# Kernel optimization log

Measured on AMD Instinct MI355X. Metric: run time of the kernel, lower is better.

Reference implementation:

```python
import jax, jax.numpy as jnp
import numpy as np
from functools import partial

HID = 256
HOR = 5

def _lin(k, i, o):
    return jax.random.normal(k, (i, o), jnp.float32) / np.sqrt(i)

def setup_inputs() -> dict:
    key = jax.random.key(0)
    ks = jax.random.split(key, 32)
    B, T, D, Hf, Wf = 4, 16, 768, 16, 16
    H, W = 1024, 1024
    inp = {}
    inp['features'] = jax.random.normal(ks[0], (B, T, D, Hf, Wf), jnp.float32)
    inp['predictions'] = jax.random.uniform(ks[1], (B, T, 1, H, W), dtype=jnp.float32)
    # position encoder: 4 -> HID -> HID
    inp['pe_w1'] = _lin(ks[2], 4, HID); inp['pe_b1'] = jnp.zeros((HID,), jnp.float32)
    inp['pe_w2'] = _lin(ks[3], HID, HID); inp['pe_b2'] = jnp.zeros((HID,), jnp.float32)
    # 2-layer LSTM, gate order i,f,g,o (torch convention)
    inp['wih0'] = _lin(ks[4], HID, 4 * HID); inp['whh0'] = _lin(ks[5], HID, 4 * HID)
    inp['bih0'] = jnp.zeros((4 * HID,), jnp.float32); inp['bhh0'] = jnp.zeros((4 * HID,), jnp.float32)
    inp['wih1'] = _lin(ks[6], HID, 4 * HID); inp['whh1'] = _lin(ks[7], HID, 4 * HID)
    inp['bih1'] = jnp.zeros((4 * HID,), jnp.float32); inp['bhh1'] = jnp.zeros((4 * HID,), jnp.float32)
    # motion predictor: HID -> HID -> HID/2 -> HOR*4
    inp['mp_w1'] = _lin(ks[8], HID, HID); inp['mp_b1'] = jnp.zeros((HID,), jnp.float32)
    inp['mp_w2'] = _lin(ks[9], HID, HID // 2); inp['mp_b2'] = jnp.zeros((HID // 2,), jnp.float32)
    inp['mp_w3'] = _lin(ks[10], HID // 2, HOR * 4); inp['mp_b3'] = jnp.zeros((HOR * 4,), jnp.float32)
    # confidence: HID -> HID/2 -> HOR
    inp['cf_w1'] = _lin(ks[11], HID, HID // 2); inp['cf_b1'] = jnp.zeros((HID // 2,), jnp.float32)
    inp['cf_w2'] = _lin(ks[12], HID // 2, HOR); inp['cf_b2'] = jnp.zeros((HOR,), jnp.float32)
    return inp

def _extract_bboxes(predictions):
    # predictions: (B,T,1,H,W) -> bboxes (B,T,4) in (cx,cy,w,h), normalized
    B, T, _, H, W = predictions.shape
    mask = predictions[:, :, 0] > 0.5  # (B,T,H,W)
    xs = jnp.arange(W, dtype=jnp.float32)           # (W,)
    ys = jnp.arange(H, dtype=jnp.float32)[:, None]  # (H,1)
    big = jnp.float32(H + W)
    x_min = jnp.min(jnp.where(mask, xs, big), axis=(-2, -1))
    x_max = jnp.max(jnp.where(mask, xs, -1.0), axis=(-2, -1))
    y_min = jnp.min(jnp.where(mask, ys, big), axis=(-2, -1))
    y_max = jnp.max(jnp.where(mask, ys, -1.0), axis=(-2, -1))
    has = jnp.any(mask, axis=(-2, -1))  # (B,T)
    cx = (x_min + x_max) / 2.0 / W
    cy = (y_min + y_max) / 2.0 / H
    w = (x_max - x_min) / W
    h = (y_max - y_min) / H
    bbox = jnp.stack([cx, cy, w, h], axis=-1)  # (B,T,4)
    default = jnp.array([0.5, 0.5, 0.1, 0.1], dtype=jnp.float32)
    return jnp.where(has[..., None], bbox, default)

def _lstm_layer(x, wih, whh, bih, bhh):
    # x: (B,T,HID); returns (hs (B,T,H), h_final (B,H))
    B = x.shape[0]
    xg = jnp.einsum('bti,ig->btg', x, wih) + bih  # (B,T,4H)
    def step(carry, xg_t):
        h, c = carry
        g = xg_t + h @ whh + bhh
        i, f, gg, o = jnp.split(g, 4, axis=-1)
        i = jax.nn.sigmoid(i); f = jax.nn.sigmoid(f)
        gg = jnp.tanh(gg); o = jax.nn.sigmoid(o)
        c = f * c + i * gg
        h = o * jnp.tanh(c)
        return (h, c), h
    z = jnp.zeros((B, HID), x.dtype)
    (h, c), hs = jax.lax.scan(step, (z, z), xg.swapaxes(0, 1))
    return hs.swapaxes(0, 1), h

def reference(features, predictions, pe_w1, pe_b1, pe_w2, pe_b2,
              wih0, whh0, bih0, bhh0, wih1, whh1, bih1, bhh1,
              mp_w1, mp_b1, mp_w2, mp_b2, mp_w3, mp_b3,
              cf_w1, cf_b1, cf_w2, cf_b2):
    B, T = features.shape[:2]
    bboxes = _extract_bboxes(predictions)  # (B,T,4)
    pos = jax.nn.relu(bboxes @ pe_w1 + pe_b1)
    pos = jax.nn.relu(pos @ pe_w2 + pe_b2)  # (B,T,HID)
    h1, _ = _lstm_layer(pos, wih0, whh0, bih0, bhh0)
    motion_features, last_hidden = _lstm_layer(h1, wih1, whh1, bih1, bhh1)
    x = jax.nn.relu(last_hidden @ mp_w1 + mp_b1)
    x = jax.nn.relu(x @ mp_w2 + mp_b2)
    predicted_deltas = (x @ mp_w3 + mp_b3).reshape(B, HOR, 4)
    last_bbox = bboxes[:, -1:, :]
    predicted_bboxes = last_bbox + jnp.cumsum(predicted_deltas, axis=1)
    c = jax.nn.relu(last_hidden @ cf_w1 + cf_b1)
    confidence = jax.nn.sigmoid(c @ cf_w2 + cf_b2)  # (B,HOR)
    predicted_locations = predicted_bboxes[..., :2]
    predicted_scales = predicted_bboxes[..., 2:]
    return (predicted_deltas, predicted_bboxes, predicted_locations,
            predicted_scales, motion_features, confidence, bboxes)
```

## Files before the change

### kernel.cpp

```cpp
#include <hip/hip_runtime.h>
#include <math.h>

#define BIGI (1 << 30)

#define PM_OFF    0
#define HT0_OFF   8192
#define HT2_OFF   40960
#define XG1_OFF   45056
#define ZERO_BEG  8192
#define ZERO_END  176128

#define OUT_DELTAS 0
#define OUT_PBB    80
#define OUT_LOC    160
#define OUT_SCL    200
#define OUT_MF     240
#define OUT_CONF   16624
#define OUT_BBOX   16644

__device__ __forceinline__ float sigmoidf_(float x) { return 1.0f / (1.0f + expf(-x)); }

__device__ __forceinline__ void storeh(unsigned long long* p, float h, int tag) {
    unsigned long long v =
        ((unsigned long long)(unsigned)tag << 32) | (unsigned long long)__float_as_uint(h);
    __hip_atomic_store(p, v, __ATOMIC_RELAXED, __HIP_MEMORY_SCOPE_AGENT);
}
__device__ __forceinline__ float pollh(const unsigned long long* p, int tag) {
    unsigned long long v = __hip_atomic_load(p, __ATOMIC_RELAXED, __HIP_MEMORY_SCOPE_AGENT);
    while ((int)(v >> 32) != tag) {
        __builtin_amdgcn_s_sleep(1);
        v = __hip_atomic_load(p, __ATOMIC_RELAXED, __HIP_MEMORY_SCOPE_AGENT);
    }
    return __uint_as_float((unsigned)v);
}

__global__ __launch_bounds__(256) void k_minmax(const float4* __restrict__ pred,
                                                int* __restrict__ ws) {
    int tid = threadIdx.x;
    {
        int i = ZERO_BEG + blockIdx.x * 256 + tid;
        if (i < ZERO_END) ws[i] = 0;
    }
    int img = blockIdx.x >> 5;
    int chunk = blockIdx.x & 31;
    int base = img * 262144 + chunk * 8192 + tid;
    int xmn = BIGI, xmx = -1, ymn = BIGI, ymx = -1;
#pragma unroll 4
    for (int i = 0; i < 32; ++i) {
        int idx4 = base + i * 256;
        float4 v = pred[idx4];
        int x = (idx4 << 2) & 1023;
        int y = (idx4 >> 8) & 1023;
        bool m0 = v.x > 0.5f, m1 = v.y > 0.5f, m2 = v.z > 0.5f, m3 = v.w > 0.5f;
        int cmn = m0 ? x : (m1 ? x + 1 : (m2 ? x + 2 : (m3 ? x + 3 : BIGI)));
        int cmx = m3 ? x + 3 : (m2 ? x + 2 : (m1 ? x + 1 : (m0 ? x : -1)));
        xmn = min(xmn, cmn);
        xmx = max(xmx, cmx);
        if (m0 | m1 | m2 | m3) { ymn = min(ymn, y); ymx = max(ymx, y); }
    }
    for (int off = 32; off > 0; off >>= 1) {
        xmn = min(xmn, __shfl_down(xmn, off));
        xmx = max(xmx, __shfl_down(xmx, off));
        ymn = min(ymn, __shfl_down(ymn, off));
        ymx = max(ymx, __shfl_down(ymx, off));
    }
    __shared__ int red[4][4];
    int wave = tid >> 6;
    if ((tid & 63) == 0) { red[0][wave] = xmn; red[1][wave] = xmx; red[2][wave] = ymn; red[3][wave] = ymx; }
    __syncthreads();
    if (tid == 0) {
        xmn = min(min(red[0][0], red[0][1]), min(red[0][2], red[0][3]));
        xmx = max(max(red[1][0], red[1][1]), max(red[1][2], red[1][3]));
        ymn = min(min(red[2][0], red[2][1]), min(red[2][2], red[2][3]));
        ymx = max(max(red[3][0], red[3][1]), max(red[3][2], red[3][3]));
        ((int4*)(ws + PM_OFF))[blockIdx.x] = make_int4(xmn, xmx, ymn, ymx);
    }
}

__device__ __forceinline__ void mk_bbox(int xmn, int xmx, int ymn, int ymx, float* o) {
    if (xmx >= 0) {
        o[0] = (float)(xmn + xmx) * (0.5f / 1024.0f);
        o[1] = (float)(ymn + ymx) * (0.5f / 1024.0f);
        o[2] = (float)(xmx - xmn) * (1.0f / 1024.0f);
        o[3] = (float)(ymx - ymn) * (1.0f / 1024.0f);
    } else { o[0] = 0.5f; o[1] = 0.5f; o[2] = 0.1f; o[3] = 0.1f; }
}

__global__ __launch_bounds__(512, 2) void k_fused(
    const float* __restrict__ pe_w1, const float* __restrict__ pe_b1,
    const float* __restrict__ pe_w2, const float* __restrict__ pe_b2,
    const float* __restrict__ wih0, const float* __restrict__ whh0,
    const float* __restrict__ bih0, const float* __restrict__ bhh0,
    const float* __restrict__ wih1, const float* __restrict__ whh1,
    const float* __restrict__ bih1, const float* __restrict__ bhh1,
    const float* __restrict__ mp_w1, const float* __restrict__ mp_b1,
    const float* __restrict__ mp_w2, const float* __restrict__ mp_b2,
    const float* __restrict__ mp_w3, const float* __restrict__ mp_b3,
    const float* __restrict__ cf_w1, const float* __restrict__ cf_b1,
    const float* __restrict__ cf_w2, const float* __restrict__ cf_b2,
    const int4* __restrict__ pm4, unsigned long long* __restrict__ hT0,
    unsigned long long* __restrict__ hT2, unsigned long long* __restrict__ xg1,
    float* __restrict__ out) {
    __shared__ __align__(16) float sA[4096];
    __shared__ __align__(16) float sB[4096];
    __shared__ __align__(16) float hsm[256];
    __shared__ float xsm[256];
    __shared__ float partA[512];
    __shared__ float sBB[64];
    const int tid = threadIdx.x, blk = blockIdx.x;
    const int stage = blk >> 4;
    const int b = (blk >> 2) & 3, g = blk & 3;
    const int c = tid & 255, kh = tid >> 8;
    const int col = ((c >> 6) << 8) + g * 64 + (c & 63);
    const int krow0 = kh * 128;

    float4 wreg[32];
    float cst = 0.0f;

    if (stage == 0) {
        {
            int il = tid >> 5, ch = tid & 31;
            int4 v = pm4[(b * 16 + il) * 32 + ch];
            int xmn = v.x, xmx = v.y, ymn = v.z, ymx = v.w;
            for (int off = 16; off > 0; off >>= 1) {
                xmn = min(xmn, __shfl_down(xmn, off, 32));
                xmx = max(xmx, __shfl_down(xmx, off, 32));
                ymn = min(ymn, __shfl_down(ymn, off, 32));
                ymx = max(ymx, __shfl_down(ymx, off, 32));
            }
            if (ch == 0) {
                float bb[4];
                mk_bbox(xmn, xmx, ymn, ymx, bb);
                sBB[il * 4 + 0] = bb[0]; sBB[il * 4 + 1] = bb[1];
                sBB[il * 4 + 2] = bb[2]; sBB[il * 4 + 3] = bb[3];
                if (g == 0) {
                    out[OUT_BBOX + (b * 16 + il) * 4 + 0] = bb[0];
                    out[OUT_BBOX + (b * 16 + il) * 4 + 1] = bb[1];
                    out[OUT_BBOX + (b * 16 + il) * 4 + 2] = bb[2];
                    out[OUT_BBOX + (b * 16 + il) * 4 + 3] = bb[3];
                }
            }
        }
        __syncthreads();
        if (tid < 256) {
            float w0 = pe_w1[tid], w1 = pe_w1[256 + tid];
            float w2 = pe_w1[512 + tid], w3 = pe_w1[768 + tid], b1v = pe_b1[tid];
#pragma unroll
            for (int i = 0; i < 16; ++i) {
                float v = sBB[i * 4] * w0 + sBB[i * 4 + 1] * w1 +
                          sBB[i * 4 + 2] * w2 + sBB[i * 4 + 3] * w3 + b1v;
                sB[i * 256 + tid] = fmaxf(v, 0.0f);
            }
        }
        __syncthreads();
        {
            int i0 = kh * 8;
            float acc[8];
            float b2v = pe_b2[c];
#pragma unroll
            for (int i = 0; i < 8; ++i) acc[i] = b2v;
            for (int k = 0; k < 256; ++k) {
                float wv = pe_w2[k * 256 + c];
#pragma unroll
                for (int i = 0; i < 8; ++i) acc[i] += sB[(i0 + i) * 256 + k] * wv;
            }
#pragma unroll
            for (int i = 0; i < 8; ++i) sA[(i0 + i) * 256 + c] = fmaxf(acc[i], 0.0f);
        }
        __syncthreads();
#pragma unroll
        for (int k4 = 0; k4 < 32; ++k4) {
            int r = krow0 + k4 * 4;
            wreg[k4].x = wih0[(r + 0) * 1024 + col];
            wreg[k4].y = wih0[(r + 1) * 1024 + col];
            wreg[k4].z = wih0[(r + 2) * 1024 + col];
            wreg[k4].w = wih0[(r + 3) * 1024 + col];
        }
        float xacc[16];
#pragma unroll
        for (int t = 0; t < 16; ++t) {
            const float4* pr = (const float4*)&sA[t * 256 + krow0];
            float a = 0.0f;
#pragma unroll
            for (int k = 0; k < 32; ++k) {
                float4 x = pr[k];
                a += x.x * wreg[k].x + x.y * wreg[k].y + x.z * wreg[k].z + x.w * wreg[k].w;
            }
            xacc[t] = a;
        }
        if (kh == 1) {
#pragma unroll
            for (int t = 0; t < 16; ++t) sB[t * 256 + c] = xacc[t];
        }
        __syncthreads();
        if (kh == 0) {
            float bsum = bih0[col] + bhh0[col];
#pragma unroll
            for (int t = 0; t < 16; ++t) sB[t * 256 + c] = xacc[t] + sB[t * 256 + c] + bsum;
        }
        __syncthreads();
#pragma unroll
        for (int k4 = 0; k4 < 32; ++k4) {
            int r = krow0 + k4 * 4;
            wreg[k4].x = whh0[(r + 0) * 1024 + col];
            wreg[k4].y = whh0[(r + 1) * 1024 + col];
            wreg[k4].z = whh0[(r + 2) * 1024 + col];
            wreg[k4].w = whh0[(r + 3) * 1024 + col];
        }
        for (int t = 0; t < 16; ++t) {
            if (t && tid < 256) hsm[tid] = pollh(&hT0[((b * 16 + t - 1) << 8) + tid], t);
            __syncthreads();
            float a = 0.0f;
            if (t) {
                const float4* hr = (const float4*)&hsm[krow0];
#pragma unroll
                for (int k = 0; k < 32; ++k) {
                    float4 h = hr[k];
                    a += h.x * wreg[k].x + h.y * wreg[k].y + h.z * wreg[k].z + h.w * wreg[k].w;
                }
            }
            partA[kh * 256 + c] = a;
            __syncthreads();
            if (tid < 64) {
                int u = tid, unit = g * 64 + u;
                float gi = sB[t * 256 + u]       + partA[u]       + partA[256 + u];
                float gf = sB[t * 256 + 64 + u]  + partA[64 + u]  + partA[320 + u];
                float gg = sB[t * 256 + 128 + u] + partA[128 + u] + partA[384 + u];
                float go = sB[t * 256 + 192 + u] + partA[192 + u] + partA[448 + u];
                float i_ = sigmoidf_(gi), f_ = sigmoidf_(gf);
                float g_ = tanhf(gg), o_ = sigmoidf_(go);
                cst = f_ * cst + i_ * g_;
                float h = o_ * tanhf(cst);
                storeh(&hT0[((b * 16 + t) << 8) + unit], h, t + 1);
            }
        }
        return;
    }

    if (stage == 1) {
#pragma unroll
        for (int k4 = 0; k4 < 32; ++k4) {
            int r = krow0 + k4 * 4;
            wreg[k4].x = wih1[(r + 0) * 1024 + col];
            wreg[k4].y = wih1[(r + 1) * 1024 + col];
            wreg[k4].z = wih1[(r + 2) * 1024 + col];
            wreg[k4].w = wih1[(r + 3) * 1024 + col];
        }
        float bsum = 0.0f;
        if (tid < 256) bsum = bih1[col] + bhh1[col];
        for (int t = 0; t < 16; ++t) {
            if (tid < 256) hsm[tid] = pollh(&hT0[((b * 16 + t) << 8) + tid], t + 1);
            __syncthreads();
            const float4* hr = (const float4*)&hsm[krow0];
            float a = 0.0f;
#pragma unroll
            for (int k = 0; k < 32; ++k) {
                float4 h = hr[k];
                a += h.x * wreg[k].x + h.y * wreg[k].y + h.z * wreg[k].z + h.w * wreg[k].w;
            }
            partA[kh * 256 + c] = a;
            __syncthreads();
            if (tid < 256) {
                float v = partA[tid] + partA[256 + tid] + bsum;
                storeh(&xg1[((b * 16 + t) << 10) + col], v, t + 1);
            }
        }
        return;
    }

#pragma unroll
    for (int k4 = 0; k4 < 32; ++k4) {
        int r = krow0 + k4 * 4;
        wreg[k4].x = whh1[(r + 0) * 1024 + col];
        wreg[k4].y = whh1[(r + 1) * 1024 + col];
        wreg[k4].z = whh1[(r + 2) * 1024 + col];
        wreg[k4].w = whh1[(r + 3) * 1024 + col];
    }
    for (int t = 0; t < 16; ++t) {
        if (tid < 256) {
            if (t) hsm[tid] = pollh(&hT2[(((b << 1) | ((t - 1) & 1)) << 8) + tid], t);
        } else {
            int cc = tid - 256;
            int colx = ((cc >> 6) << 8) + g * 64 + (cc & 63);
            xsm[cc] = pollh(&xg1[((b * 16 + t) << 10) + colx], t + 1);
        }
        __syncthreads();
        float a = 0.0f;
        if (t) {
            const float4* hr = (const float4*)&hsm[krow0];
#pragma unroll
            for (int k = 0; k < 32; ++k) {
                float4 h = hr[k];
                a += h.x * wreg[k].x + h.y * wreg[k].y + h.z * wreg[k].z + h.w * wreg[k].w;
            }
        }
        partA[kh * 256 + c] = a;
        __syncthreads();
        if (tid < 64) {
            int u = tid, unit = g * 64 + u;
            float gi = xsm[u]       + partA[u]       + partA[256 + u];
            float gf = xsm[64 + u]  + partA[64 + u]  + partA[320 + u];
            float gg = xsm[128 + u] + partA[128 + u] + partA[384 + u];
            float go = xsm[192 + u] + partA[192 + u] + partA[448 + u];
            float i_ = sigmoidf_(gi), f_ = sigmoidf_(gf);
            float g_ = tanhf(gg), o_ = sigmoidf_(go);
            cst = f_ * cst + i_ * g_;
            float h = o_ * tanhf(cst);
            storeh(&hT2[(((b << 1) | (t & 1)) << 8) + unit], h, t + 1);
            out[OUT_MF + (b * 16 + t) * 256 + unit] = h;
        }
    }
    if (g != 0) return;

    float* lh = sA;
    float* x1 = sA + 256;
    float* c1 = sA + 512;
    float* x2 = sA + 640;
    float* dl = sA + 768;
    if (tid < 256) lh[tid] = pollh(&hT2[(((b << 1) | 1) << 8) + tid], 16);
    if (tid < 32) {
        int4 v = pm4[(b * 16 + 15) * 32 + tid];
        int xmn = v.x, xmx = v.y, ymn = v.z, ymx = v.w;
        for (int off = 16; off > 0; off >>= 1) {
            xmn = min(xmn, __shfl_down(xmn, off, 32));
            xmx = max(xmx, __shfl_down(xmx, off, 32));
            ymn = min(ymn, __shfl_down(ymn, off, 32));
            ymx = max(ymx, __shfl_down(ymx, off, 32));
        }
        if (tid == 0) mk_bbox(xmn, xmx, ymn, ymx, sBB);
    }
    __syncthreads();
    if (tid < 256) {
        float a = mp_b1[tid];
#pragma unroll 4
        for (int k = 0; k < 256; ++k) a += lh[k] * mp_w1[k * 256 + tid];
        x1[tid] = fmaxf(a, 0.0f);
    } else if (tid < 384) {
        int jj = tid - 256;
        float a = cf_b1[jj];
#pragma unroll 4
        for (int k = 0; k < 256; ++k) a += lh[k] * cf_w1[k * 128 + jj];
        c1[jj] = fmaxf(a, 0.0f);
    }
    __syncthreads();
    if (tid < 128) {
        float a = mp_b2[tid];
#pragma unroll 4
        for (int k = 0; k < 256; ++k) a += x1[k] * mp_w2[k * 128 + tid];
        x2[tid] = fmaxf(a, 0.0f);
    } else if (tid >= 256 && tid < 261) {
        int jj = tid - 256;
        float a = cf_b2[jj];
#pragma unroll 4
        for (int k = 0; k < 128; ++k) a += c1[k] * cf_w2[k * 5 + jj];
        out[OUT_CONF + b * 5 + jj] = sigmoidf_(a);
    }
    __syncthreads();
    if (tid < 20) {
        float a = mp_b3[tid];
#pragma unroll 4
        for (int k = 0; k < 128; ++k) a += x2[k] * mp_w3[k * 20 + tid];
        dl[tid] = a;
        out[OUT_DELTAS + b * 20 + tid] = a;
    }
    __syncthreads();
    if (tid < 4) {
        float acc = sBB[tid];
        for (int hh = 0; hh < 5; ++hh) {
            acc += dl[hh * 4 + tid];
            out[OUT_PBB + b * 20 + hh * 4 + tid] = acc;
            if (tid < 2) out[OUT_LOC + b * 10 + hh * 2 + tid] = acc;
            else out[OUT_SCL + b * 10 + hh * 2 + (tid - 2)] = acc;
        }
    }
}

extern "C" void kernel_launch(void* const* d_in, const int* in_sizes, int n_in,
                              void* d_out, int out_size, void* d_ws, size_t ws_size,
                              hipStream_t stream) {
    (void)in_sizes; (void)n_in; (void)out_size; (void)ws_size;
    const float* pred = (const float*)d_in[1];
    const float* pe_w1 = (const float*)d_in[2];
    const float* pe_b1 = (const float*)d_in[3];
    const float* pe_w2 = (const float*)d_in[4];
    const float* pe_b2 = (const float*)d_in[5];
    const float* wih0 = (const float*)d_in[6];
    const float* whh0 = (const float*)d_in[7];
    const float* bih0 = (const float*)d_in[8];
    const float* bhh0 = (const float*)d_in[9];
    const float* wih1 = (const float*)d_in[10];
    const float* whh1 = (const float*)d_in[11];
    const float* bih1 = (const float*)d_in[12];
    const float* bhh1 = (const float*)d_in[13];
    const float* mp_w1 = (const float*)d_in[14];
    const float* mp_b1 = (const float*)d_in[15];
    const float* mp_w2 = (const float*)d_in[16];
    const float* mp_b2 = (const float*)d_in[17];
    const float* mp_w3 = (const float*)d_in[18];
    const float* mp_b3 = (const float*)d_in[19];
    const float* cf_w1 = (const float*)d_in[20];
    const float* cf_b1 = (const float*)d_in[21];
    const float* cf_w2 = (const float*)d_in[22];
    const float* cf_b2 = (const float*)d_in[23];
    float* out = (float*)d_out;
    int* wsi = (int*)d_ws;

    hipLaunchKernelGGL(k_minmax, dim3(64 * 32), dim3(256), 0, stream,
                       (const float4*)pred, wsi);
    hipLaunchKernelGGL(k_fused, dim3(48), dim3(512), 0, stream,
                       pe_w1, pe_b1, pe_w2, pe_b2,
                       wih0, whh0, bih0, bhh0,
                       wih1, whh1, bih1, bhh1,
                       mp_w1, mp_b1, mp_w2, mp_b2, mp_w3, mp_b3,
                       cf_w1, cf_b1, cf_w2, cf_b2,
                       (const int4*)(wsi + PM_OFF),
                       (unsigned long long*)(wsi + HT0_OFF),
                       (unsigned long long*)(wsi + HT2_OFF),
                       (unsigned long long*)(wsi + XG1_OFF),
                       out);
}
```

Baseline: 559.5 us.

## Split fused LSTM kernel across twice as many smaller blocks per batch

Repartitions the fused LSTM pipeline from 48 blocks of 512 threads to 96 blocks of 256 threads, each owning 32 hidden units per gate instead of 64. The K dimension is still split into two halves across threads, and the per-block gate work, shared buffers and bbox reduction are resized to match. Layer-1 x-gates and the recurrent hidden state are now polled together in one helper, and the confidence head is moved into otherwise idle threads. The aim is more CUs working on each recurrent step with less work per block, at the cost of more cross-block polling traffic and more blocks to synchronise each timestep.

New measurement: 570.0 us. About the same (+1.9%).

```diff
diff --git a/kernel.cpp b/kernel.cpp
--- a/kernel.cpp
+++ b/kernel.cpp
@@ -32,6 +32,20 @@
         v = __hip_atomic_load(p, __ATOMIC_RELAXED, __HIP_MEMORY_SCOPE_AGENT);
     }
     return __uint_as_float((unsigned)v);
+}
+__device__ __forceinline__ float2 pollh2(const unsigned long long* p1, int tag1,
+                                         const unsigned long long* p2, int tag2) {
+    unsigned long long v1 = __hip_atomic_load(p1, __ATOMIC_RELAXED, __HIP_MEMORY_SCOPE_AGENT);
+    unsigned long long v2 = __hip_atomic_load(p2, __ATOMIC_RELAXED, __HIP_MEMORY_SCOPE_AGENT);
+    while ((int)(v1 >> 32) != tag1) {
+        __builtin_amdgcn_s_sleep(1);
+        v1 = __hip_atomic_load(p1, __ATOMIC_RELAXED, __HIP_MEMORY_SCOPE_AGENT);
+    }
+    while ((int)(v2 >> 32) != tag2) {
+        __builtin_amdgcn_s_sleep(1);
+        v2 = __hip_atomic_load(p2, __ATOMIC_RELAXED, __HIP_MEMORY_SCOPE_AGENT);
+    }
+    return make_float2(__uint_as_float((unsigned)v1), __uint_as_float((unsigned)v2));
 }
 
 __global__ __launch_bounds__(256) void k_minmax(const float4* __restrict__ pred,
@@ -86,7 +100,7 @@
     } else { o[0] = 0.5f; o[1] = 0.5f; o[2] = 0.1f; o[3] = 0.1f; }
 }
 
-__global__ __launch_bounds__(512, 2) void k_fused(
+__global__ __launch_bounds__(256, 1) void k_fused(
     const float* __restrict__ pe_w1, const float* __restrict__ pe_b1,
     const float* __restrict__ pe_w2, const float* __restrict__ pe_b2,
     const float* __restrict__ wih0, const float* __restrict__ whh0,
@@ -103,15 +117,16 @@
     float* __restrict__ out) {
     __shared__ __align__(16) float sA[4096];
     __shared__ __align__(16) float sB[4096];
+    __shared__ float xgl[2048];
     __shared__ __align__(16) float hsm[256];
-    __shared__ float xsm[256];
-    __shared__ float partA[512];
+    __shared__ float xsm[128];
+    __shared__ float part[256];
     __shared__ float sBB[64];
     const int tid = threadIdx.x, blk = blockIdx.x;
-    const int stage = blk >> 4;
-    const int b = (blk >> 2) & 3, g = blk & 3;
-    const int c = tid & 255, kh = tid >> 8;
-    const int col = ((c >> 6) << 8) + g * 64 + (c & 63);
+    const int stage = blk >> 5;
+    const int b = (blk >> 3) & 3, g = blk & 7;
+    const int j = tid & 127, kh = tid >> 7;
+    const int col = ((j >> 5) << 8) + g * 32 + (j & 31);
     const int krow0 = kh * 128;
 
     float4 wreg[32];
@@ -119,16 +134,18 @@
 
     if (stage == 0) {
         {
-            int il = tid >> 5, ch = tid & 31;
-            int4 v = pm4[(b * 16 + il) * 32 + ch];
-            int xmn = v.x, xmx = v.y, ymn = v.z, ymx = v.w;
-            for (int off = 16; off > 0; off >>= 1) {
-                xmn = min(xmn, __shfl_down(xmn, off, 32));
-                xmx = max(xmx, __shfl_down(xmx, off, 32));
-                ymn = min(ymn, __shfl_down(ymn, off, 32));
-                ymx = max(ymx, __shfl_down(ymx, off, 32));
-            }
-            if (ch == 0) {
+            int il = tid >> 4, c2 = (tid & 15) * 2;
+            int4 A = pm4[(b * 16 + il) * 32 + c2];
+            int4 B = pm4[(b * 16 + il) * 32 + c2 + 1];
+            int xmn = min(A.x, B.x), xmx = max(A.y, B.y);
+            int ymn = min(A.z, B.z), ymx = max(A.w, B.w);
+            for (int off = 8; off > 0; off >>= 1) {
+                xmn = min(xmn, __shfl_down(xmn, off, 16));
+                xmx = max(xmx, __shfl_down(xmx, off, 16));
+                ymn = min(ymn, __shfl_down(ymn, off, 16));
+                ymx = max(ymx, __shfl_down(ymx, off, 16));
+            }
+            if ((tid & 15) == 0) {
                 float bb[4];
                 mk_bbox(xmn, xmx, ymn, ymx, bb);
                 sBB[il * 4 + 0] = bb[0]; sBB[il * 4 + 1] = bb[1];
@@ -142,7 +159,7 @@
             }
         }
         __syncthreads();
-        if (tid < 256) {
+        {
             float w0 = pe_w1[tid], w1 = pe_w1[256 + tid];
             float w2 = pe_w1[512 + tid], w3 = pe_w1[768 + tid], b1v = pe_b1[tid];
 #pragma unroll
@@ -154,18 +171,17 @@
         }
         __syncthreads();
         {
-            int i0 = kh * 8;
-            float acc[8];
-            float b2v = pe_b2[c];
-#pragma unroll
-            for (int i = 0; i < 8; ++i) acc[i] = b2v;
+            float acc[16];
+            float b2v = pe_b2[tid];
+#pragma unroll
+            for (int i = 0; i < 16; ++i) acc[i] = b2v;
             for (int k = 0; k < 256; ++k) {
-                float wv = pe_w2[k * 256 + c];
-#pragma unroll
-                for (int i = 0; i < 8; ++i) acc[i] += sB[(i0 + i) * 256 + k] * wv;
-            }
-#pragma unroll
-            for (int i = 0; i < 8; ++i) sA[(i0 + i) * 256 + c] = fmaxf(acc[i], 0.0f);
+                float wv = pe_w2[k * 256 + tid];
+#pragma unroll
+                for (int i = 0; i < 16; ++i) acc[i] += sB[i * 256 + k] * wv;
+            }
+#pragma unroll
+            for (int i = 0; i < 16; ++i) sA[i * 256 + tid] = fmaxf(acc[i], 0.0f);
         }
         __syncthreads();
 #pragma unroll
@@ -176,29 +192,31 @@
             wreg[k4].z = wih0[(r + 2) * 1024 + col];
             wreg[k4].w = wih0[(r + 3) * 1024 + col];
         }
-        float xacc[16];
-#pragma unroll
-        for (int t = 0; t < 16; ++t) {
-            const float4* pr = (const float4*)&sA[t * 256 + krow0];
-            float a = 0.0f;
-#pragma unroll
-            for (int k = 0; k < 32; ++k) {
-                float4 x = pr[k];
-                a += x.x * wreg[k].x + x.y * wreg[k].y + x.z * wreg[k].z + x.w * wreg[k].w;
-            }
-            xacc[t] = a;
-        }
-        if (kh == 1) {
-#pragma unroll
-            for (int t = 0; t < 16; ++t) sB[t * 256 + c] = xacc[t];
-        }
-        __syncthreads();
-        if (kh == 0) {
+        {
+            float xacc[16];
+#pragma unroll
+            for (int t = 0; t < 16; ++t) {
+                const float4* pr = (const float4*)&sA[t * 256 + krow0];
+                float a = 0.0f;
+#pragma unroll
+                for (int k = 0; k < 32; ++k) {
+                    float4 x = pr[k];
+                    a += x.x * wreg[k].x + x.y * wreg[k].y + x.z * wreg[k].z + x.w * wreg[k].w;
+                }
+                xacc[t] = a;
+            }
+#pragma unroll
+            for (int t = 0; t < 16; ++t) sB[kh * 2048 + t * 128 + j] = xacc[t];
+        }
+        __syncthreads();
+        {
             float bsum = bih0[col] + bhh0[col];
-#pragma unroll
-            for (int t = 0; t < 16; ++t) sB[t * 256 + c] = xacc[t] + sB[t * 256 + c] + bsum;
-        }
-        __syncthreads();
+            int th = tid >> 7;
+            for (int i = 0; i < 8; ++i) {
+                int t = th + 2 * i;
+                xgl[t * 128 + j] = sB[t * 128 + j] + sB[2048 + t * 128 + j] + bsum;
+            }
+        }
 #pragma unroll
         for (int k4 = 0; k4 < 32; ++k4) {
             int r = krow0 + k4 * 4;
@@ -207,8 +225,9 @@
             wreg[k4].z = whh0[(r + 2) * 1024 + col];
             wreg[k4].w = whh0[(r + 3) * 1024 + col];
         }
+        __syncthreads();
         for (int t = 0; t < 16; ++t) {
-            if (t && tid < 256) hsm[tid] = pollh(&hT0[((b * 16 + t - 1) << 8) + tid], t);
+            if (t) hsm[tid] = pollh(&hT0[((b * 16 + t - 1) << 8) + tid], t);
             __syncthreads();
             float a = 0.0f;
             if (t) {
@@ -219,19 +238,19 @@
                     a += h.x * wreg[k].x + h.y * wreg[k].y + h.z * wreg[k].z + h.w * wreg[k].w;
                 }
             }
-            partA[kh * 256 + c] = a;
+            part[tid] = a;
             __syncthreads();
-            if (tid < 64) {
-                int u = tid, unit = g * 64 + u;
-                float gi = sB[t * 256 + u]       + partA[u]       + partA[256 + u];
-                float gf = sB[t * 256 + 64 + u]  + partA[64 + u]  + partA[320 + u];
-                float gg = sB[t * 256 + 128 + u] + partA[128 + u] + partA[384 + u];
-                float go = sB[t * 256 + 192 + u] + partA[192 + u] + partA[448 + u];
+            if (tid < 32) {
+                int u = tid;
+                float gi = xgl[t * 128 + u]      + part[u]       + part[128 + u];
+                float gf = xgl[t * 128 + 32 + u] + part[32 + u]  + part[160 + u];
+                float gg = xgl[t * 128 + 64 + u] + part[64 + u]  + part[192 + u];
+                float go = xgl[t * 128 + 96 + u] + part[96 + u]  + part[224 + u];
                 float i_ = sigmoidf_(gi), f_ = sigmoidf_(gf);
                 float g_ = tanhf(gg), o_ = sigmoidf_(go);
                 cst = f_ * cst + i_ * g_;
                 float h = o_ * tanhf(cst);
-                storeh(&hT0[((b * 16 + t) << 8) + unit], h, t + 1);
+                storeh(&hT0[((b * 16 + t) << 8) + g * 32 + u], h, t + 1);
             }
         }
         return;
@@ -246,10 +265,9 @@
             wreg[k4].z = wih1[(r + 2) * 1024 + col];
             wreg[k4].w = wih1[(r + 3) * 1024 + col];
         }
-        float bsum = 0.0f;
-        if (tid < 256) bsum = bih1[col] + bhh1[col];
+        float bsum = (tid < 128) ? (bih1[col] + bhh1[col]) : 0.0f;
         for (int t = 0; t < 16; ++t) {
-            if (tid < 256) hsm[tid] = pollh(&hT0[((b * 16 + t) << 8) + tid], t + 1);
+            hsm[tid] = pollh(&hT0[((b * 16 + t) << 8) + tid], t + 1);
             __syncthreads();
             const float4* hr = (const float4*)&hsm[krow0];
             float a = 0.0f;
@@ -258,12 +276,10 @@
                 float4 h = hr[k];
                 a += h.x * wreg[k].x + h.y * wreg[k].y + h.z * wreg[k].z + h.w * wreg[k].w;
             }
-            partA[kh * 256 + c] = a;
+            part[tid] = a;
             __syncthreads();
-            if (tid < 256) {
-                float v = partA[tid] + partA[256 + tid] + bsum;
-                storeh(&xg1[((b * 16 + t) << 10) + col], v, t + 1);
-            }
+            if (tid < 128)
+                storeh(&xg1[((b * 16 + t) << 10) + col], part[tid] + part[128 + tid] + bsum, t + 1);
         }
         return;
     }
@@ -277,12 +293,16 @@
         wreg[k4].w = whh1[(r + 3) * 1024 + col];
     }
     for (int t = 0; t < 16; ++t) {
-        if (tid < 256) {
-            if (t) hsm[tid] = pollh(&hT2[(((b << 1) | ((t - 1) & 1)) << 8) + tid], t);
-        } else {
-            int cc = tid - 256;
-            int colx = ((cc >> 6) << 8) + g * 64 + (cc & 63);
-            xsm[cc] = pollh(&xg1[((b * 16 + t) << 10) + colx], t + 1);
+        if (tid < 128) {
+            if (t) {
+                float2 v = pollh2(&xg1[((b * 16 + t) << 10) + col], t + 1,
+                                  &hT2[(((b << 1) | ((t - 1) & 1)) << 8) + tid], t);
+                xsm[tid] = v.x; hsm[tid] = v.y;
+            } else {
+                xsm[tid] = pollh(&xg1[((b * 16) << 10) + col], 1);
+            }
+        } else if (t) {
+            hsm[tid] = pollh(&hT2[(((b << 1) | ((t - 1) & 1)) << 8) + tid], t);
         }
         __syncthreads();
         float a = 0.0f;
@@ -294,14 +314,14 @@
                 a += h.x * wreg[k].x + h.y * wreg[k].y + h.z * wreg[k].z + h.w * wreg[k].w;
             }
         }
-        partA[kh * 256 + c] = a;
-        __syncthreads();
-        if (tid < 64) {
-            int u = tid, unit = g * 64 + u;
-            float gi = xsm[u]       + partA[u]       + partA[256 + u];
-            float gf = xsm[64 + u]  + partA[64 + u]  + partA[320 + u];
-            float gg = xsm[128 + u] + partA[128 + u] + partA[384 + u];
-            float go = xsm[192 + u] + partA[192 + u] + partA[448 + u];
+        part[tid] = a;
+        __syncthreads();
+        if (tid < 32) {
+            int u = tid, unit = g * 32 + u;
+            float gi = xsm[u]      + part[u]       + part[128 + u];
+            float gf = xsm[32 + u] + part[32 + u]  + part[160 + u];
+            float gg = xsm[64 + u] + part[64 + u]  + part[192 + u];
+            float go = xsm[96 + u] + part[96 + u]  + part[224 + u];
             float i_ = sigmoidf_(gi), f_ = sigmoidf_(gf);
             float g_ = tanhf(gg), o_ = sigmoidf_(go);
             cst = f_ * cst + i_ * g_;
@@ -317,7 +337,7 @@
     float* c1 = sA + 512;
     float* x2 = sA + 640;
     float* dl = sA + 768;
-    if (tid < 256) lh[tid] = pollh(&hT2[(((b << 1) | 1) << 8) + tid], 16);
+    lh[tid] = pollh(&hT2[(((b << 1) | 1) << 8) + tid], 16);
     if (tid < 32) {
         int4 v = pm4[(b * 16 + 15) * 32 + tid];
         int xmn = v.x, xmx = v.y, ymn = v.z, ymx = v.w;
@@ -330,17 +350,11 @@
         if (tid == 0) mk_bbox(xmn, xmx, ymn, ymx, sBB);
     }
     __syncthreads();
-    if (tid < 256) {
+    {
         float a = mp_b1[tid];
 #pragma unroll 4
         for (int k = 0; k < 256; ++k) a += lh[k] * mp_w1[k * 256 + tid];
         x1[tid] = fmaxf(a, 0.0f);
-    } else if (tid < 384) {
-        int jj = tid - 256;
-        float a = cf_b1[jj];
-#pragma unroll 4
-        for (int k = 0; k < 256; ++k) a += lh[k] * cf_w1[k * 128 + jj];
-        c1[jj] = fmaxf(a, 0.0f);
     }
     __syncthreads();
     if (tid < 128) {
@@ -348,12 +362,12 @@
 #pragma unroll 4
         for (int k = 0; k < 256; ++k) a += x1[k] * mp_w2[k * 128 + tid];
         x2[tid] = fmaxf(a, 0.0f);
-    } else if (tid >= 256 && tid < 261) {
-        int jj = tid - 256;
-        float a = cf_b2[jj];
-#pragma unroll 4
-        for (int k = 0; k < 128; ++k) a += c1[k] * cf_w2[k * 5 + jj];
-        out[OUT_CONF + b * 5 + jj] = sigmoidf_(a);
+    } else {
+        int jj = tid - 128;
+        float a = cf_b1[jj];
+#pragma unroll 4
+        for (int k = 0; k < 256; ++k) a += lh[k] * cf_w1[k * 128 + jj];
+        c1[jj] = fmaxf(a, 0.0f);
     }
     __syncthreads();
     if (tid < 20) {
@@ -362,6 +376,12 @@
         for (int k = 0; k < 128; ++k) a += x2[k] * mp_w3[k * 20 + tid];
         dl[tid] = a;
         out[OUT_DELTAS + b * 20 + tid] = a;
+    } else if (tid >= 32 && tid < 37) {
+        int idx = tid - 32;
+        float a = cf_b2[idx];
+#pragma unroll 4
+        for (int k = 0; k < 128; ++k) a += c1[k] * cf_w2[k * 5 + idx];
+        out[OUT_CONF + b * 5 + idx] = sigmoidf_(a);
     }
     __syncthreads();
     if (tid < 4) {
@@ -407,7 +427,7 @@
 
     hipLaunchKernelGGL(k_minmax, dim3(64 * 32), dim3(256), 0, stream,
                        (const float4*)pred, wsi);
-    hipLaunchKernelGGL(k_fused, dim3(48), dim3(512), 0, stream,
+    hipLaunchKernelGGL(k_fused, dim3(96), dim3(256), 0, stream,
                        pe_w1, pe_b1, pe_w2, pe_b2,
                        wih0, whh0, bih0, bhh0,
                        wih1, whh1, bih1, bhh1,
```
